# Performance work log

Hardware: AMD Instinct MI355X
Metric: run time of the kernel (lower is better)

## Reference

```python
import jax, jax.numpy as jnp
import numpy as np

N0, N1, N2 = 200000, 100000, 50000
DEG = 16
E0, E1 = N1 * DEG, N2 * DEG
EP = 500000
IN, H, EDGE_IN, MLP_H, NCLS = 64, 128, 16, 128, 8
EPS = 1e-5  # BatchNorm eps


def setup_inputs() -> dict:
    key = jax.random.key(0)
    ks = jax.random.split(key, 22)
    def w(k, shape, fan_in):
        return jax.random.normal(k, shape, dtype=jnp.float32) * (1.0 / np.sqrt(fan_in))
    inp = {
        'x_nodes': jax.random.normal(ks[0], (N0, IN), dtype=jnp.float32),
        'src0': jax.random.randint(ks[1], (E0,), 0, N0, dtype=jnp.int32),
        'dst0': jax.random.randint(ks[2], (E0,), 0, N1, dtype=jnp.int32),
        'src1': jax.random.randint(ks[3], (E1,), 0, N1, dtype=jnp.int32),
        'dst1': jax.random.randint(ks[4], (E1,), 0, N2, dtype=jnp.int32),
        'u': jax.random.randint(ks[5], (EP,), 0, N2, dtype=jnp.int32),
        'v': jax.random.randint(ks[6], (EP,), 0, N2, dtype=jnp.int32),
        'e_feat': jax.random.normal(ks[7], (EP, EDGE_IN), dtype=jnp.float32),
        # SAGEConv layer 0 (DGL mean aggregator: fc_self(h_dst) + fc_neigh(mean_neigh) + bias)
        'Ws0': w(ks[8], (IN, H), IN), 'Wn0': w(ks[9], (IN, H), IN), 'b0': jnp.zeros((H,), jnp.float32),
        'g0': jnp.ones((H,), jnp.float32), 'be0': jnp.zeros((H,), jnp.float32),
        # SAGEConv layer 1
        'Ws1': w(ks[10], (H, H), H), 'Wn1': w(ks[11], (H, H), H), 'b1': jnp.zeros((H,), jnp.float32),
        'g1': jnp.ones((H,), jnp.float32), 'be1': jnp.zeros((H,), jnp.float32),
        # edge MLP: Linear(2H+edge_in, MLP_H) -> ReLU -> (Dropout eval=no-op) -> Linear(MLP_H, NCLS)
        'W1': w(ks[12], (2 * H + EDGE_IN, MLP_H), 2 * H + EDGE_IN), 'bm1': jnp.zeros((MLP_H,), jnp.float32),
        'W2': w(ks[13], (MLP_H, NCLS), MLP_H), 'bm2': jnp.zeros((NCLS,), jnp.float32),
    }
    return inp


def _sage_mean(h_src, src, dst, num_dst, Ws, Wn, b):
    # gather neighbor feats, segment-mean over dst, then linear combine
    msgs = h_src[src]                                            # [E, d]
    agg = jax.ops.segment_sum(msgs, dst, num_segments=num_dst)   # [num_dst, d]
    deg = jax.ops.segment_sum(jnp.ones((src.shape[0],), h_src.dtype), dst, num_segments=num_dst)
    mean = agg / jnp.maximum(deg, 1.0)[:, None]
    h_dst = h_src[:num_dst]
    return h_dst @ Ws + mean @ Wn + b


def _bn_relu(x, gamma, beta):
    # training-mode BatchNorm1d over rows, followed by ReLU
    mu = x.mean(axis=0)
    var = x.var(axis=0)
    return jax.nn.relu(gamma * (x - mu) * jax.lax.rsqrt(var + EPS) + beta)


def reference(x_nodes, src0, dst0, src1, dst1, u, v, e_feat,
              Ws0, Wn0, b0, g0, be0, Ws1, Wn1, b1, g1, be1, W1, bm1, W2, bm2):
    h = _bn_relu(_sage_mean(x_nodes, src0, dst0, N1, Ws0, Wn0, b0), g0, be0)  # [N1, H]
    h = _bn_relu(_sage_mean(h, src1, dst1, N2, Ws1, Wn1, b1), g1, be1)        # [N2, H]
    e_repr = jnp.concatenate([h[u], h[v], e_feat], axis=1)                    # [EP, 2H+edge_in]
    hidden = jax.nn.relu(e_repr @ W1 + bm1)
    return hidden @ W2 + bm2                                                  # [EP, NCLS]
```

## Files before the change

kernel.cpp:

```cpp
#include <hip/hip_runtime.h>
#include <hip/hip_bf16.h>

#define CN0 200000
#define CN1 100000
#define CN2 50000
#define CE0 1600000
#define CE1 800000
#define CEP 500000
#define CIN 64
#define CH  128
#define CEIN 16
#define CMH 128
#define CNCLS 8

typedef __bf16 bf16x8 __attribute__((ext_vector_type(8)));
typedef float  f32x4  __attribute__((ext_vector_type(4)));
typedef unsigned short u16x8 __attribute__((ext_vector_type(8)));
typedef unsigned short u16x4 __attribute__((ext_vector_type(4)));

__device__ inline float b2f(unsigned short u) {
  union { unsigned int i; float f; } x; x.i = ((unsigned int)u) << 16; return x.f;
}
__device__ inline unsigned short f2bu(float f) {
  __hip_bfloat16 h = __float2bfloat16(f);
  return *reinterpret_cast<unsigned short*>(&h);
}

__global__ void k_hist(const int* __restrict__ dst, int n, int* __restrict__ cnt) {
  int i = blockIdx.x * blockDim.x + threadIdx.x;
  if (i < n) atomicAdd(&cnt[dst[i]], 1);
}

__global__ __launch_bounds__(256) void k_scan1(const int* __restrict__ cnt, int n,
                                               int* __restrict__ excl, int* __restrict__ bsum) {
  __shared__ int sh[256];
  int t = threadIdx.x;
  int base = blockIdx.x * 1024 + t * 4;
  int v[4];
#pragma unroll
  for (int i = 0; i < 4; i++) v[i] = (base + i < n) ? cnt[base + i] : 0;
  int tsum = v[0] + v[1] + v[2] + v[3];
  sh[t] = tsum; __syncthreads();
  for (int ofs = 1; ofs < 256; ofs <<= 1) {
    int x = (t >= ofs) ? sh[t - ofs] : 0; __syncthreads();
    sh[t] += x; __syncthreads();
  }
  int run = sh[t] - tsum;
  if (t == 255) bsum[blockIdx.x] = sh[255];
#pragma unroll
  for (int i = 0; i < 4; i++) {
    if (base + i < n) excl[base + i] = run;
    run += v[i];
  }
}

__global__ __launch_bounds__(256) void k_scan2(int* __restrict__ bsum, int n) {
  __shared__ int sh[256];
  int t = threadIdx.x;
  int v = (t < n) ? bsum[t] : 0;
  sh[t] = v; __syncthreads();
  for (int ofs = 1; ofs < 256; ofs <<= 1) {
    int x = (t >= ofs) ? sh[t - ofs] : 0; __syncthreads();
    sh[t] += x; __syncthreads();
  }
  if (t < n) bsum[t] = sh[t] - v;
}

__global__ void k_scan3(int* __restrict__ off, int* __restrict__ cur,
                        const int* __restrict__ bsum, int n, int total) {
  int i = blockIdx.x * blockDim.x + threadIdx.x;
  if (i < n) {
    int vv = off[i] + bsum[i >> 10];
    off[i] = vv; cur[i] = vv;
  }
  if (i == n) off[n] = total;
}

__global__ void k_reorder(const int* __restrict__ src, const int* __restrict__ dst,
                          int n, int* __restrict__ cur, int* __restrict__ srcs) {
  int i = blockIdx.x * blockDim.x + threadIdx.x;
  if (i < n) {
    int p = atomicAdd(&cur[dst[i]], 1);
    srcs[p] = src[i];
  }
}

__global__ __launch_bounds__(256) void k_gather64b(
    const __hip_bfloat16* __restrict__ xb, const int* __restrict__ off,
    const int* __restrict__ srcs, __hip_bfloat16* __restrict__ meanb, int nnodes) {
  int node = blockIdx.x * 4 + (threadIdx.x >> 6);
  if (node >= nnodes) return;
  int lane = threadIdx.x & 63;
  int g = lane >> 3;
  int f8 = (lane & 7) * 8;
  int s = off[node], e = off[node + 1];
  float acc[8] = {0.f,0.f,0.f,0.f,0.f,0.f,0.f,0.f};
  for (int p = s + g; p < e; p += 8) {
    int sn = srcs[p];
    u16x8 v = *reinterpret_cast<const u16x8*>(xb + (long long)sn * CIN + f8);
#pragma unroll
    for (int j = 0; j < 8; j++) acc[j] += b2f(v[j]);
  }
#pragma unroll
  for (int m = 8; m < 64; m <<= 1)
#pragma unroll
    for (int j = 0; j < 8; j++) acc[j] += __shfl_xor(acc[j], m, 64);
  if (g == 0) {
    float inv = 1.0f / (float)max(e - s, 1);
    u16x8 o;
#pragma unroll
    for (int j = 0; j < 8; j++) o[j] = f2bu(acc[j] * inv);
    *reinterpret_cast<u16x8*>(meanb + (long long)node * CIN + f8) = o;
  }
}

__global__ __launch_bounds__(256) void k_gather128b(
    const __hip_bfloat16* __restrict__ hb, const int* __restrict__ off,
    const int* __restrict__ srcs, __hip_bfloat16* __restrict__ meanb, int nnodes) {
  int node = blockIdx.x * 4 + (threadIdx.x >> 6);
  if (node >= nnodes) return;
  int lane = threadIdx.x & 63;
  int g = lane >> 4;
  int f8 = (lane & 15) * 8;
  int s = off[node], e = off[node + 1];
  float acc[8] = {0.f,0.f,0.f,0.f,0.f,0.f,0.f,0.f};
  for (int p = s + g; p < e; p += 4) {
    int sn = srcs[p];
    u16x8 v = *reinterpret_cast<const u16x8*>(hb + (long long)sn * CH + f8);
#pragma unroll
    for (int j = 0; j < 8; j++) acc[j] += b2f(v[j]);
  }
#pragma unroll
  for (int m = 16; m < 64; m <<= 1)
#pragma unroll
    for (int j = 0; j < 8; j++) acc[j] += __shfl_xor(acc[j], m, 64);
  if (g == 0) {
    float inv = 1.0f / (float)max(e - s, 1);
    u16x8 o;
#pragma unroll
    for (int j = 0; j < 8; j++) o[j] = f2bu(acc[j] * inv);
    *reinterpret_cast<u16x8*>(meanb + (long long)node * CH + f8) = o;
  }
}

template<int KA>
__global__ __launch_bounds__(256) void k_sage_mfma(
    const __hip_bfloat16* __restrict__ A1, const __hip_bfloat16* __restrict__ A2,
    const __hip_bfloat16* __restrict__ wT, const float* __restrict__ bias,
    __hip_bfloat16* __restrict__ outb, int M) {
  int tid = threadIdx.x;
  int lane = tid & 63;
  int w = tid >> 6;
  int wm = w & 1, wn = w >> 1;
  int l15 = lane & 15, lk = lane >> 4;
  int r0 = blockIdx.x * 64;

  int rA = r0 + wm * 32 + l15;
  int rB = rA + 16;
  int rAc = min(rA, M - 1), rBc = min(rB, M - 1);
  const __hip_bfloat16* a1A = A1 + (long long)rAc * KA + lk * 8;
  const __hip_bfloat16* a1B = A1 + (long long)rBc * KA + lk * 8;
  const __hip_bfloat16* a2A = A2 + (long long)rAc * KA + lk * 8;
  const __hip_bfloat16* a2B = A2 + (long long)rBc * KA + lk * 8;
  const __hip_bfloat16* wp[4];
#pragma unroll
  for (int nf = 0; nf < 4; nf++)
    wp[nf] = wT + (long long)(wn * 64 + nf * 16 + l15) * (2 * KA) + lk * 8;

  f32x4 acc[2][4];
#pragma unroll
  for (int nf = 0; nf < 4; nf++) {
    float bv = bias[wn * 64 + nf * 16 + l15];
#pragma unroll
    for (int m = 0; m < 2; m++) {
      acc[m][nf][0] = bv; acc[m][nf][1] = bv;
      acc[m][nf][2] = bv; acc[m][nf][3] = bv;
    }
  }

  constexpr int HS = KA / 32;
#pragma unroll
  for (int kk = 0; kk < 2 * HS; kk++) {
    bf16x8 a0, a1v;
    if (kk < HS) {
      a0  = *reinterpret_cast<const bf16x8*>(a1A + kk * 32);
      a1v = *reinterpret_cast<const bf16x8*>(a1B + kk * 32);
    } else {
      a0  = *reinterpret_cast<const bf16x8*>(a2A + (kk - HS) * 32);
      a1v = *reinterpret_cast<const bf16x8*>(a2B + (kk - HS) * 32);
    }
#pragma unroll
    for (int nf = 0; nf < 4; nf++) {
      bf16x8 b = *reinterpret_cast<const bf16x8*>(wp[nf] + kk * 32);
      acc[0][nf] = __builtin_amdgcn_mfma_f32_16x16x32_bf16(a0,  b, acc[0][nf], 0, 0, 0);
      acc[1][nf] = __builtin_amdgcn_mfma_f32_16x16x32_bf16(a1v, b, acc[1][nf], 0, 0, 0);
    }
  }

  unsigned short* ob = reinterpret_cast<unsigned short*>(outb);
#pragma unroll
  for (int m = 0; m < 2; m++)
#pragma unroll
    for (int nf = 0; nf < 4; nf++)
#pragma unroll
      for (int r = 0; r < 4; r++) {
        int row = r0 + wm * 32 + m * 16 + lk * 4 + r;
        if (row < M) ob[(long long)row * CH + wn * 64 + nf * 16 + l15] = f2bu(acc[m][nf][r]);
      }
}

__global__ __launch_bounds__(256) void k_colstats_b(
    const __hip_bfloat16* __restrict__ h, int nrows, float* __restrict__ stats) {
  int tid = threadIdx.x;
  int lane = tid & 63;
  int wv = tid >> 6;
  int cg = lane & 15;
  float s[8] = {0,0,0,0,0,0,0,0}, ss[8] = {0,0,0,0,0,0,0,0};
  for (int r = blockIdx.x * 16 + (tid >> 4); r < nrows; r += gridDim.x * 16) {
    u16x8 v = *reinterpret_cast<const u16x8*>(h + (long long)r * CH + cg * 8);
#pragma unroll
    for (int j = 0; j < 8; j++) { float f = b2f(v[j]); s[j] += f; ss[j] = fmaf(f, f, ss[j]); }
  }
#pragma unroll
  for (int m = 16; m < 64; m <<= 1)
#pragma unroll
    for (int j = 0; j < 8; j++) { s[j] += __shfl_xor(s[j], m, 64); ss[j] += __shfl_xor(ss[j], m, 64); }
  __shared__ float red[2][4][16][8];
  if (lane < 16) {
#pragma unroll
    for (int j = 0; j < 8; j++) { red[0][wv][lane][j] = s[j]; red[1][wv][lane][j] = ss[j]; }
  }
  __syncthreads();
  if (tid < 128) {
    int c = tid >> 3, j = tid & 7;
    float a = red[0][0][c][j] + red[0][1][c][j] + red[0][2][c][j] + red[0][3][c][j];
    float b = red[1][0][c][j] + red[1][1][c][j] + red[1][2][c][j] + red[1][3][c][j];
    atomicAdd(&stats[c * 8 + j], a);
    atomicAdd(&stats[CH + c * 8 + j], b);
  }
}

__global__ void k_bnrelu_b(__hip_bfloat16* __restrict__ h, int nrows,
                           const float* __restrict__ stats,
                           const float* __restrict__ g, const float* __restrict__ be) {
  int total8 = nrows * (CH / 8);
  float inv_n = 1.0f / (float)nrows;
  for (int i = blockIdx.x * blockDim.x + threadIdx.x; i < total8;
       i += gridDim.x * blockDim.x) {
    int cg = (i & 15) * 8;
    u16x8 v = reinterpret_cast<u16x8*>(h)[i];
    u16x8 o;
#pragma unroll
    for (int j = 0; j < 8; j++) {
      int c = cg + j;
      float mu = stats[c] * inv_n;
      float var = stats[CH + c] * inv_n - mu * mu;
      float rs = rsqrtf(var + 1e-5f);
      float val = (b2f(v[j]) - mu) * rs * g[c] + be[c];
      o[j] = f2bu(fmaxf(val, 0.0f));
    }
    reinterpret_cast<u16x8*>(h)[i] = o;
  }
}

__global__ void k_f2b4(const float* __restrict__ src, __hip_bfloat16* __restrict__ dst, int n4) {
  for (int i = blockIdx.x * blockDim.x + threadIdx.x; i < n4; i += gridDim.x * blockDim.x) {
    float4 v = reinterpret_cast<const float4*>(src)[i];
    u16x4 o; o[0] = f2bu(v.x); o[1] = f2bu(v.y); o[2] = f2bu(v.z); o[3] = f2bu(v.w);
    reinterpret_cast<u16x4*>(dst)[i] = o;
  }
}

__global__ void k_prep(const float* __restrict__ Ws0, const float* __restrict__ Wn0,
                       const float* __restrict__ Ws1, const float* __restrict__ Wn1,
                       const float* __restrict__ W1,
                       __hip_bfloat16* __restrict__ wT0, __hip_bfloat16* __restrict__ wT1,
                       __hip_bfloat16* __restrict__ w1t) {
  int t = blockIdx.x * blockDim.x + threadIdx.x;
  if (t < 16384) {
    int n = t >> 7, k = t & 127;
    wT0[t] = __float2bfloat16(k < 64 ? Ws0[k * CH + n] : Wn0[(k - 64) * CH + n]);
    return;
  }
  t -= 16384;
  if (t < 32768) {
    int n = t >> 8, k = t & 255;
    wT1[t] = __float2bfloat16(k < 128 ? Ws1[k * CH + n] : Wn1[(k - 128) * CH + n]);
    return;
  }
  t -= 32768;
  if (t < 34816) {
    int n = t / 272, k = t % 272;
    w1t[t] = __float2bfloat16(W1[k * CMH + n]);
  }
}

__global__ __launch_bounds__(256) void k_edge_mfma(
    const __hip_bfloat16* __restrict__ h2b, const int* __restrict__ u,
    const int* __restrict__ v, const float* __restrict__ ef,
    const __hip_bfloat16* __restrict__ w1t, const float* __restrict__ bm1,
    const float* __restrict__ W2, const float* __restrict__ bm2,
    float* __restrict__ out) {
  __shared__ unsigned short hid[64][136];
  int tid = threadIdx.x;
  int lane = tid & 63;
  int w = tid >> 6;
  int wm = w & 1;
  int wn = w >> 1;
  int l15 = lane & 15, lk = lane >> 4;
  int e0 = blockIdx.x * 64;

  int eA = e0 + wm * 32 + l15;
  int eB = eA + 16;
  int eAc = min(eA, CEP - 1), eBc = min(eB, CEP - 1);
  int uA = u[eAc], uB = u[eBc], vA = v[eAc], vB = v[eBc];

  const __hip_bfloat16* auP = h2b + (long long)uA * CH + lk * 8;
  const __hip_bfloat16* buP = h2b + (long long)uB * CH + lk * 8;
  const __hip_bfloat16* avP = h2b + (long long)vA * CH + lk * 8;
  const __hip_bfloat16* bvP = h2b + (long long)vB * CH + lk * 8;

  const __hip_bfloat16* wb[4];
#pragma unroll
  for (int nf = 0; nf < 4; nf++)
    wb[nf] = w1t + (long long)(wn * 64 + nf * 16 + l15) * (2 * CH + CEIN) + lk * 8;

  bf16x8 zf = {};
  bf16x8 aefA = zf, aefB = zf;
  if (lk < 2) {
    const float* pA = ef + (long long)eAc * CEIN + lk * 8;
    const float* pB = ef + (long long)eBc * CEIN + lk * 8;
    u16x8 ua, ub;
#pragma unroll
    for (int j = 0; j < 8; j++) { ua[j] = f2bu(pA[j]); ub[j] = f2bu(pB[j]); }
    aefA = *reinterpret_cast<bf16x8*>(&ua);
    aefB = *reinterpret_cast<bf16x8*>(&ub);
  }

  f32x4 acc[2][4];
#pragma unroll
  for (int nf = 0; nf < 4; nf++) {
    float bias = bm1[wn * 64 + nf * 16 + l15];
#pragma unroll
    for (int m = 0; m < 2; m++) {
      acc[m][nf][0] = bias; acc[m][nf][1] = bias;
      acc[m][nf][2] = bias; acc[m][nf][3] = bias;
    }
  }

#pragma unroll
  for (int kk = 0; kk < 9; kk++) {
    bf16x8 a0, a1;
    if (kk < 4) {
      a0 = *reinterpret_cast<const bf16x8*>(auP + kk * 32);
      a1 = *reinterpret_cast<const bf16x8*>(buP + kk * 32);
    } else if (kk < 8) {
      a0 = *reinterpret_cast<const bf16x8*>(avP + (kk - 4) * 32);
      a1 = *reinterpret_cast<const bf16x8*>(bvP + (kk - 4) * 32);
    } else {
      a0 = aefA;
      a1 = aefB;
    }
#pragma unroll
    for (int nf = 0; nf < 4; nf++) {
      bf16x8 b;
      if (kk < 8) b = *reinterpret_cast<const bf16x8*>(wb[nf] + kk * 32);
      else        b = (lk < 2) ? *reinterpret_cast<const bf16x8*>(wb[nf] + 256) : zf;
      acc[0][nf] = __builtin_amdgcn_mfma_f32_16x16x32_bf16(a0, b, acc[0][nf], 0, 0, 0);
      acc[1][nf] = __builtin_amdgcn_mfma_f32_16x16x32_bf16(a1, b, acc[1][nf], 0, 0, 0);
    }
  }

#pragma unroll
  for (int m = 0; m < 2; m++)
#pragma unroll
    for (int nf = 0; nf < 4; nf++)
#pragma unroll
      for (int r = 0; r < 4; r++) {
        int row = wm * 32 + m * 16 + lk * 4 + r;
        int col = wn * 64 + nf * 16 + l15;
        hid[row][col] = f2bu(fmaxf(acc[m][nf][r], 0.0f));
      }
  __syncthreads();

#pragma unroll
  for (int i = tid; i < 64 * CNCLS; i += 256) {
    int e = i >> 3, c = i & 7;
    if (e0 + e >= CEP) continue;
    float o = bm2[c];
    const u16x8* hp = reinterpret_cast<const u16x8*>(&hid[e][0]);
#pragma unroll
    for (int k8 = 0; k8 < 16; k8++) {
      u16x8 hv = hp[k8];
#pragma unroll
      for (int j = 0; j < 8; j++)
        o = fmaf(b2f(hv[j]), W2[(k8 * 8 + j) * CNCLS + c], o);
    }
    out[(long long)(e0 + e) * CNCLS + c] = o;
  }
}

extern "C" void kernel_launch(void* const* d_in, const int* in_sizes, int n_in,
                              void* d_out, int out_size, void* d_ws, size_t ws_size,
                              hipStream_t stream) {
  const float* x_nodes = (const float*)d_in[0];
  const int*   src0    = (const int*)d_in[1];
  const int*   dst0    = (const int*)d_in[2];
  const int*   src1    = (const int*)d_in[3];
  const int*   dst1    = (const int*)d_in[4];
  const int*   u       = (const int*)d_in[5];
  const int*   v       = (const int*)d_in[6];
  const float* e_feat  = (const float*)d_in[7];
  const float* Ws0     = (const float*)d_in[8];
  const float* Wn0     = (const float*)d_in[9];
  const float* b0      = (const float*)d_in[10];
  const float* g0      = (const float*)d_in[11];
  const float* be0     = (const float*)d_in[12];
  const float* Ws1     = (const float*)d_in[13];
  const float* Wn1     = (const float*)d_in[14];
  const float* b1      = (const float*)d_in[15];
  const float* g1      = (const float*)d_in[16];
  const float* be1     = (const float*)d_in[17];
  const float* W1      = (const float*)d_in[18];
  const float* bm1     = (const float*)d_in[19];
  const float* W2      = (const float*)d_in[20];
  const float* bm2     = (const float*)d_in[21];
  float* out = (float*)d_out;

  float* ws = (float*)d_ws;
  __hip_bfloat16* xb    = (__hip_bfloat16*)(ws + 0);
  __hip_bfloat16* h2b   = (__hip_bfloat16*)(ws + 0);
  __hip_bfloat16* meanb = (__hip_bfloat16*)(ws + 6400000);
  __hip_bfloat16* h1b   = (__hip_bfloat16*)(ws + 9600000);
  __hip_bfloat16* wT0   = (__hip_bfloat16*)(ws + 16000000);
  __hip_bfloat16* wT1   = (__hip_bfloat16*)(ws + 16010000);
  __hip_bfloat16* w1tb  = (__hip_bfloat16*)(ws + 16030000);
  float* s0   = ws + 16050000;
  float* s1   = ws + 16050256;
  int*   offA = (int*)(ws + 16060000);
  int*   curA = (int*)(ws + 16170000);
  int*   cntA = (int*)(ws + 16280000);
  int*   bsum = (int*)(ws + 16390000);
  int*   srcs = (int*)(ws + 16400000);

  hipMemsetAsync(s0, 0, 512 * sizeof(float), stream);
  k_prep<<<(16384 + 32768 + 34816 + 255) / 256, 256, 0, stream>>>(
      Ws0, Wn0, Ws1, Wn1, W1, wT0, wT1, w1tb);
  k_f2b4<<<2048, 256, 0, stream>>>(x_nodes, xb, CN0 * CIN / 4);

  hipMemsetAsync(cntA, 0, CN1 * sizeof(int), stream);
  k_hist<<<(CE0 + 255) / 256, 256, 0, stream>>>(dst0, CE0, cntA);
  {
    int nblk = (CN1 + 1023) / 1024;
    k_scan1<<<nblk, 256, 0, stream>>>(cntA, CN1, offA, bsum);
    k_scan2<<<1, 256, 0, stream>>>(bsum, nblk);
    k_scan3<<<(CN1 + 256) / 256, 256, 0, stream>>>(offA, curA, bsum, CN1, CE0);
  }
  k_reorder<<<(CE0 + 255) / 256, 256, 0, stream>>>(src0, dst0, CE0, curA, srcs);

  k_gather64b<<<(CN1 + 3) / 4, 256, 0, stream>>>(xb, offA, srcs, meanb, CN1);
  k_sage_mfma<CIN><<<(CN1 + 63) / 64, 256, 0, stream>>>(xb, meanb, wT0, b0, h1b, CN1);
  k_colstats_b<<<256, 256, 0, stream>>>(h1b, CN1, s0);
  k_bnrelu_b<<<2048, 256, 0, stream>>>(h1b, CN1, s0, g0, be0);

  hipMemsetAsync(cntA, 0, CN2 * sizeof(int), stream);
  k_hist<<<(CE1 + 255) / 256, 256, 0, stream>>>(dst1, CE1, cntA);
  {
    int nblk = (CN2 + 1023) / 1024;
    k_scan1<<<nblk, 256, 0, stream>>>(cntA, CN2, offA, bsum);
    k_scan2<<<1, 256, 0, stream>>>(bsum, nblk);
    k_scan3<<<(CN2 + 256) / 256, 256, 0, stream>>>(offA, curA, bsum, CN2, CE1);
  }
  k_reorder<<<(CE1 + 255) / 256, 256, 0, stream>>>(src1, dst1, CE1, curA, srcs);

  k_gather128b<<<(CN2 + 3) / 4, 256, 0, stream>>>(h1b, offA, srcs, meanb, CN2);
  k_sage_mfma<CH><<<(CN2 + 63) / 64, 256, 0, stream>>>(h1b, meanb, wT1, b1, h2b, CN2);
  k_colstats_b<<<256, 256, 0, stream>>>(h2b, CN2, s1);
  k_bnrelu_b<<<2048, 256, 0, stream>>>(h2b, CN2, s1, g1, be1);

  k_edge_mfma<<<(CEP + 63) / 64, 256, 0, stream>>>(h2b, u, v, e_feat, w1tb, bm1, W2, bm2, out);
}
```

Baseline: 800.1 us.

## Fuse BN column stats into SAGE GEMM and use MFMA for second edge layer

```diff
diff --git a/kernel.cpp b/kernel.cpp
--- a/kernel.cpp
+++ b/kernel.cpp
@@ -147,13 +147,16 @@
 __global__ __launch_bounds__(256) void k_sage_mfma(
     const __hip_bfloat16* __restrict__ A1, const __hip_bfloat16* __restrict__ A2,
     const __hip_bfloat16* __restrict__ wT, const float* __restrict__ bias,
-    __hip_bfloat16* __restrict__ outb, int M) {
+    __hip_bfloat16* __restrict__ outb, float* __restrict__ stats, int M) {
+  __shared__ float ssum[CH], ssq[CH];
   int tid = threadIdx.x;
   int lane = tid & 63;
   int w = tid >> 6;
   int wm = w & 1, wn = w >> 1;
   int l15 = lane & 15, lk = lane >> 4;
   int r0 = blockIdx.x * 64;
+
+  if (tid < CH) { ssum[tid] = 0.f; ssq[tid] = 0.f; }
 
   int rA = r0 + wm * 32 + l15;
   int rB = rA + 16;
@@ -196,47 +199,34 @@
       acc[1][nf] = __builtin_amdgcn_mfma_f32_16x16x32_bf16(a1v, b, acc[1][nf], 0, 0, 0);
     }
   }
+  __syncthreads();
 
   unsigned short* ob = reinterpret_cast<unsigned short*>(outb);
 #pragma unroll
-  for (int m = 0; m < 2; m++)
-#pragma unroll
-    for (int nf = 0; nf < 4; nf++)
+  for (int nf = 0; nf < 4; nf++) {
+    float cs = 0.f, cq = 0.f;
+#pragma unroll
+    for (int m = 0; m < 2; m++)
 #pragma unroll
       for (int r = 0; r < 4; r++) {
         int row = r0 + wm * 32 + m * 16 + lk * 4 + r;
-        if (row < M) ob[(long long)row * CH + wn * 64 + nf * 16 + l15] = f2bu(acc[m][nf][r]);
+        if (row < M) {
+          float v = acc[m][nf][r];
+          cs += v; cq = fmaf(v, v, cq);
+          ob[(long long)row * CH + wn * 64 + nf * 16 + l15] = f2bu(v);
+        }
       }
-}
-
-__global__ __launch_bounds__(256) void k_colstats_b(
-    const __hip_bfloat16* __restrict__ h, int nrows, float* __restrict__ stats) {
-  int tid = threadIdx.x;
-  int lane = tid & 63;
-  int wv = tid >> 6;
-  int cg = lane & 15;
-  float s[8] = {0,0,0,0,0,0,0,0}, ss[8] = {0,0,0,0,0,0,0,0};
-  for (int r = blockIdx.x * 16 + (tid >> 4); r < nrows; r += gridDim.x * 16) {
-    u16x8 v = *reinterpret_cast<const u16x8*>(h + (long long)r * CH + cg * 8);
-#pragma unroll
-    for (int j = 0; j < 8; j++) { float f = b2f(v[j]); s[j] += f; ss[j] = fmaf(f, f, ss[j]); }
-  }
-#pragma unroll
-  for (int m = 16; m < 64; m <<= 1)
-#pragma unroll
-    for (int j = 0; j < 8; j++) { s[j] += __shfl_xor(s[j], m, 64); ss[j] += __shfl_xor(ss[j], m, 64); }
-  __shared__ float red[2][4][16][8];
-  if (lane < 16) {
-#pragma unroll
-    for (int j = 0; j < 8; j++) { red[0][wv][lane][j] = s[j]; red[1][wv][lane][j] = ss[j]; }
+    cs += __shfl_xor(cs, 16, 64); cq += __shfl_xor(cq, 16, 64);
+    cs += __shfl_xor(cs, 32, 64); cq += __shfl_xor(cq, 32, 64);
+    if (lk == 0) {
+      atomicAdd(&ssum[wn * 64 + nf * 16 + l15], cs);
+      atomicAdd(&ssq [wn * 64 + nf * 16 + l15], cq);
+    }
   }
   __syncthreads();
-  if (tid < 128) {
-    int c = tid >> 3, j = tid & 7;
-    float a = red[0][0][c][j] + red[0][1][c][j] + red[0][2][c][j] + red[0][3][c][j];
-    float b = red[1][0][c][j] + red[1][1][c][j] + red[1][2][c][j] + red[1][3][c][j];
-    atomicAdd(&stats[c * 8 + j], a);
-    atomicAdd(&stats[CH + c * 8 + j], b);
+  if (tid < CH) {
+    atomicAdd(&stats[tid], ssum[tid]);
+    atomicAdd(&stats[CH + tid], ssq[tid]);
   }
 }
 
@@ -273,9 +263,9 @@
 
 __global__ void k_prep(const float* __restrict__ Ws0, const float* __restrict__ Wn0,
                        const float* __restrict__ Ws1, const float* __restrict__ Wn1,
-                       const float* __restrict__ W1,
+                       const float* __restrict__ W1, const float* __restrict__ W2,
                        __hip_bfloat16* __restrict__ wT0, __hip_bfloat16* __restrict__ wT1,
-                       __hip_bfloat16* __restrict__ w1t) {
+                       __hip_bfloat16* __restrict__ w1t, __hip_bfloat16* __restrict__ w2t) {
   int t = blockIdx.x * blockDim.x + threadIdx.x;
   if (t < 16384) {
     int n = t >> 7, k = t & 127;
@@ -292,6 +282,12 @@
   if (t < 34816) {
     int n = t / 272, k = t % 272;
     w1t[t] = __float2bfloat16(W1[k * CMH + n]);
+    return;
+  }
+  t -= 34816;
+  if (t < 2048) {
+    int c = t >> 7, k = t & 127;
+    w2t[t] = __float2bfloat16(c < CNCLS ? W2[k * CNCLS + c] : 0.0f);
   }
 }
 
@@ -299,9 +295,9 @@
     const __hip_bfloat16* __restrict__ h2b, const int* __restrict__ u,
     const int* __restrict__ v, const float* __restrict__ ef,
     const __hip_bfloat16* __restrict__ w1t, const float* __restrict__ bm1,
-    const float* __restrict__ W2, const float* __restrict__ bm2,
+    const __hip_bfloat16* __restrict__ w2t, const float* __restrict__ bm2,
     float* __restrict__ out) {
-  __shared__ unsigned short hid[64][136];
+  __shared__ __align__(16) unsigned short hid[64][152];
   int tid = threadIdx.x;
   int lane = tid & 63;
   int w = tid >> 6;
@@ -330,9 +326,15 @@
   if (lk < 2) {
     const float* pA = ef + (long long)eAc * CEIN + lk * 8;
     const float* pB = ef + (long long)eBc * CEIN + lk * 8;
+    float4 a0 = *reinterpret_cast<const float4*>(pA);
+    float4 a1 = *reinterpret_cast<const float4*>(pA + 4);
+    float4 b0 = *reinterpret_cast<const float4*>(pB);
+    float4 b1 = *reinterpret_cast<const float4*>(pB + 4);
     u16x8 ua, ub;
-#pragma unroll
-    for (int j = 0; j < 8; j++) { ua[j] = f2bu(pA[j]); ub[j] = f2bu(pB[j]); }
+    ua[0]=f2bu(a0.x); ua[1]=f2bu(a0.y); ua[2]=f2bu(a0.z); ua[3]=f2bu(a0.w);
+    ua[4]=f2bu(a1.x); ua[5]=f2bu(a1.y); ua[6]=f2bu(a1.z); ua[7]=f2bu(a1.w);
+    ub[0]=f2bu(b0.x); ub[1]=f2bu(b0.y); ub[2]=f2bu(b0.z); ub[3]=f2bu(b0.w);
+    ub[4]=f2bu(b1.x); ub[5]=f2bu(b1.y); ub[6]=f2bu(b1.z); ub[7]=f2bu(b1.w);
     aefA = *reinterpret_cast<bf16x8*>(&ua);
     aefB = *reinterpret_cast<bf16x8*>(&ub);
   }
@@ -383,20 +385,25 @@
       }
   __syncthreads();
 
-#pragma unroll
-  for (int i = tid; i < 64 * CNCLS; i += 256) {
-    int e = i >> 3, c = i & 7;
-    if (e0 + e >= CEP) continue;
-    float o = bm2[c];
-    const u16x8* hp = reinterpret_cast<const u16x8*>(&hid[e][0]);
-#pragma unroll
-    for (int k8 = 0; k8 < 16; k8++) {
-      u16x8 hv = hp[k8];
-#pragma unroll
-      for (int j = 0; j < 8; j++)
-        o = fmaf(b2f(hv[j]), W2[(k8 * 8 + j) * CNCLS + c], o);
-    }
-    out[(long long)(e0 + e) * CNCLS + c] = o;
+  {
+    int we = w * 16;
+    const __hip_bfloat16* w2p = w2t + (long long)l15 * CMH + lk * 8;
+    float bv2 = (l15 < CNCLS) ? bm2[l15] : 0.0f;
+    f32x4 o; o[0] = bv2; o[1] = bv2; o[2] = bv2; o[3] = bv2;
+#pragma unroll
+    for (int kk = 0; kk < 4; kk++) {
+      bf16x8 a = *reinterpret_cast<const bf16x8*>(
+          reinterpret_cast<const unsigned short*>(&hid[we + l15][0]) + kk * 32 + lk * 8);
+      bf16x8 b = *reinterpret_cast<const bf16x8*>(w2p + kk * 32);
+      o = __builtin_amdgcn_mfma_f32_16x16x32_bf16(a, b, o, 0, 0, 0);
+    }
+    if (l15 < CNCLS) {
+#pragma unroll
+      for (int r = 0; r < 4; r++) {
+        int e = e0 + we + lk * 4 + r;
+        if (e < CEP) out[(long long)e * CNCLS + l15] = o[r];
+      }
+    }
   }
 }
 
@@ -435,6 +442,7 @@
   __hip_bfloat16* wT0   = (__hip_bfloat16*)(ws + 16000000);
   __hip_bfloat16* wT1   = (__hip_bfloat16*)(ws + 16010000);
   __hip_bfloat16* w1tb  = (__hip_bfloat16*)(ws + 16030000);
+  __hip_bfloat16* w2tb  = (__hip_bfloat16*)(ws + 16048000);
   float* s0   = ws + 16050000;
   float* s1   = ws + 16050256;
   int*   offA = (int*)(ws + 16060000);
@@ -444,8 +452,8 @@
   int*   srcs = (int*)(ws + 16400000);
 
   hipMemsetAsync(s0, 0, 512 * sizeof(float), stream);
-  k_prep<<<(16384 + 32768 + 34816 + 255) / 256, 256, 0, stream>>>(
-      Ws0, Wn0, Ws1, Wn1, W1, wT0, wT1, w1tb);
+  k_prep<<<(16384 + 32768 + 34816 + 2048 + 255) / 256, 256, 0, stream>>>(
+      Ws0, Wn0, Ws1, Wn1, W1, W2, wT0, wT1, w1tb, w2tb);
   k_f2b4<<<2048, 256, 0, stream>>>(x_nodes, xb, CN0 * CIN / 4);
 
   hipMemsetAsync(cntA, 0, CN1 * sizeof(int), stream);
@@ -459,8 +467,7 @@
   k_reorder<<<(CE0 + 255) / 256, 256, 0, stream>>>(src0, dst0, CE0, curA, srcs);
 
   k_gather64b<<<(CN1 + 3) / 4, 256, 0, stream>>>(xb, offA, srcs, meanb, CN1);
-  k_sage_mfma<CIN><<<(CN1 + 63) / 64, 256, 0, stream>>>(xb, meanb, wT0, b0, h1b, CN1);
-  k_colstats_b<<<256, 256, 0, stream>>>(h1b, CN1, s0);
+  k_sage_mfma<CIN><<<(CN1 + 63) / 64, 256, 0, stream>>>(xb, meanb, wT0, b0, h1b, s0, CN1);
   k_bnrelu_b<<<2048, 256, 0, stream>>>(h1b, CN1, s0, g0, be0);
 
   hipMemsetAsync(cntA, 0, CN2 * sizeof(int), stream);
@@ -474,9 +481,8 @@
   k_reorder<<<(CE1 + 255) / 256, 256, 0, stream>>>(src1, dst1, CE1, curA, srcs);
 
   k_gather128b<<<(CN2 + 3) / 4, 256, 0, stream>>>(h1b, offA, srcs, meanb, CN2);
-  k_sage_mfma<CH><<<(CN2 + 63) / 64, 256, 0, stream>>>(h1b, meanb, wT1, b1, h2b, CN2);
-  k_colstats_b<<<256, 256, 0, stream>>>(h2b, CN2, s1);
+  k_sage_mfma<CH><<<(CN2 + 63) / 64, 256, 0, stream>>>(h1b, meanb, wT1, b1, h2b, s1, CN2);
   k_bnrelu_b<<<2048, 256, 0, stream>>>(h2b, CN2, s1, g1, be1);
 
-  k_edge_mfma<<<(CEP + 63) / 64, 256, 0, stream>>>(h2b, u, v, e_feat, w1tb, bm1, W2, bm2, out);
-}
+  k_edge_mfma<<<(CEP + 63) / 64, 256, 0, stream>>>(h2b, u, v, e_feat, w1tb, bm1, w2tb, bm2, out);
+}
```

After: 781.7 us. 2.3% less time.
